# Kernel tuning notes

Hardware: AMD Instinct MI355X
Metric: run time of the kernel (lower is better)

## Reference

```python
import jax, jax.numpy as jnp
import numpy as np
from jax import lax


def ternarize(w):
    """Standard TWN ternarization with straight-through estimator.
    delta = 0.7*mean(|w|); alpha = mean(|w|) over kept entries; w_t = alpha*sign(w)*mask.
    """
    a = jnp.abs(w)
    delta = 0.7 * a.mean()
    mask = (a > delta).astype(w.dtype)
    alpha = (a * mask).sum() / jnp.maximum(mask.sum(), 1.0)
    wt = alpha * jnp.sign(w) * mask
    return w + lax.stop_gradient(wt - w)  # STE


def conv3x3(x, w, b):
    y = lax.conv_general_dilated(x, ternarize(w), window_strides=(1, 1),
                                 padding=((1, 1), (1, 1)),
                                 dimension_numbers=('NCHW', 'OIHW', 'NCHW'))
    return y + b[None, :, None, None]


def maxpool2(x):
    return lax.reduce_window(x, -jnp.inf, lax.max, (1, 1, 2, 2), (1, 1, 2, 2), 'VALID')


def setup_inputs() -> dict:
    key = jax.random.key(0)
    ks = jax.random.split(key, 11)
    s = lambda k, shape, scale: jax.random.normal(k, shape, dtype=jnp.float32) * scale
    return {
        'x':   s(ks[0], (1024, 3, 32, 32), 1.0),
        'w1':  s(ks[1], (64, 3, 3, 3), 0.1),
        'b1':  s(ks[2], (64,), 0.01),
        'w2':  s(ks[3], (128, 64, 3, 3), 0.05),
        'b2':  s(ks[4], (128,), 0.01),
        'w3':  s(ks[5], (256, 128, 3, 3), 0.03),
        'b3':  s(ks[6], (256,), 0.01),
        'wf1': s(ks[7], (256, 4096), 0.02),
        'bf1': s(ks[8], (256,), 0.01),
        'wf2': s(ks[9], (10, 256), 0.06),
        'bf2': s(ks[10], (10,), 0.01),
    }


def reference(x, w1, b1, w2, b2, w3, b3, wf1, bf1, wf2, bf2):
    x = maxpool2(jax.nn.relu(conv3x3(x, w1, b1)))   # [B,64,16,16]
    x = maxpool2(jax.nn.relu(conv3x3(x, w2, b2)))   # [B,128,8,8]
    x = maxpool2(jax.nn.relu(conv3x3(x, w3, b3)))   # [B,256,4,4]
    x = x.reshape(-1, 256 * 4 * 4)
    x = jax.nn.relu(x @ ternarize(wf1).T + bf1)     # [B,256]
    return x @ ternarize(wf2).T + bf2               # [B,10]
```

## Files before the change

### kernel.cpp

```cpp
#include <hip/hip_runtime.h>
#include <hip/hip_bf16.h>


typedef __attribute__((ext_vector_type(8))) short short8;
typedef __attribute__((ext_vector_type(4))) float f32x4;
typedef __attribute__((ext_vector_type(4))) int i32x4;

__device__ __forceinline__ unsigned short f2bf(float x) {
    unsigned u = __float_as_uint(x);
    return (unsigned short)((u + 0x7fffu + ((u >> 16) & 1u)) >> 16);
}
__device__ __forceinline__ float bf2f(unsigned short b) {
    return __uint_as_float(((unsigned)b) << 16);
}

#define WS_W1B   0
#define N_W1B    2048
#define WS_W2P   (WS_W1B + N_W1B)
#define N_W2P    (9*128*64)
#define WS_W3P   (WS_W2P + N_W2P)
#define N_W3P    (9*256*128)
#define WS_WTF1  (WS_W3P + N_W3P)
#define N_WTF1   (256*4096)
#define WS_WTF2  (WS_WTF1 + N_WTF1)
#define N_WTF2   (10*256)
#define WS_A1    (WS_WTF2 + N_WTF2)
#define N_A1     (1024*256*64)
#define WS_A2    (WS_A1 + N_A1)
#define N_A2     (1024*64*128)
#define WS_A3    (WS_A2 + N_A2)
#define N_A3     (1024*16*256)
#define WS_F1    (WS_A3 + N_A3)
#define N_F1     (1024*256)
#define WS_SCR   (WS_F1 + N_F1)

#define FC1_S    16

struct TernArgs {
    const float* w[6];
    int n[6];
};

__global__ void tern_stats1(TernArgs ta, double* __restrict__ scr) {
    const int wi = blockIdx.y;
    const float* __restrict__ w = ta.w[wi];
    const int n = ta.n[wi];
    __shared__ double red[4];
    const int lane = threadIdx.x & 63, wv = threadIdx.x >> 6;
    if (wi == 5) {
        float m = 0.f;
        for (int i = blockIdx.x * blockDim.x + threadIdx.x; i < n;
             i += gridDim.x * blockDim.x)
            m = fmaxf(m, fabsf(w[i]));
        #pragma unroll
        for (int off = 32; off > 0; off >>= 1)
            m = fmaxf(m, __shfl_down(m, off, 64));
        if (lane == 0) red[wv] = (double)m;
        __syncthreads();
        if (threadIdx.x == 0) {
            float mm = (float)fmax(fmax(red[0], red[1]), fmax(red[2], red[3]));
            atomicMax((int*)(scr + 20), __float_as_int(mm));
        }
        return;
    }
    double s = 0.0;
    for (int i = blockIdx.x * blockDim.x + threadIdx.x; i < n;
         i += gridDim.x * blockDim.x)
        s += (double)fabsf(w[i]);
    #pragma unroll
    for (int off = 32; off > 0; off >>= 1) s += __shfl_down(s, off, 64);
    if (lane == 0) red[wv] = s;
    __syncthreads();
    if (threadIdx.x == 0)
        atomicAdd(scr + wi * 4, red[0] + red[1] + red[2] + red[3]);
}

__global__ void tern_stats2(TernArgs ta, double* __restrict__ scr) {
    const int wi = blockIdx.y;
    const float* __restrict__ w = ta.w[wi];
    const int n = ta.n[wi];
    const float delta = (float)(0.7 * scr[wi * 4] / (double)n);
    double ms = 0.0, cnt = 0.0;
    for (int i = blockIdx.x * blockDim.x + threadIdx.x; i < n;
         i += gridDim.x * blockDim.x) {
        float a = fabsf(w[i]);
        if (a > delta) { ms += (double)a; cnt += 1.0; }
    }
    #pragma unroll
    for (int off = 32; off > 0; off >>= 1) {
        ms += __shfl_down(ms, off, 64);
        cnt += __shfl_down(cnt, off, 64);
    }
    __shared__ double redm[4], redc[4];
    const int lane = threadIdx.x & 63, wv = threadIdx.x >> 6;
    if (lane == 0) { redm[wv] = ms; redc[wv] = cnt; }
    __syncthreads();
    if (threadIdx.x == 0) {
        atomicAdd(scr + wi * 4 + 1, redm[0] + redm[1] + redm[2] + redm[3]);
        atomicAdd(scr + wi * 4 + 2, redc[0] + redc[1] + redc[2] + redc[3]);
    }
}

__global__ void tern_write_all(TernArgs ta, const double* __restrict__ scr,
                               signed char* __restrict__ w1b,
                               signed char* __restrict__ w2p8,
                               signed char* __restrict__ w3p8,
                               unsigned short* __restrict__ wtf1b,
                               float* __restrict__ wtf2) {
    const int wi = blockIdx.y;
    const float* __restrict__ w = ta.w[wi];
    const int n = ta.n[wi];
    const double* sc = scr + wi * 4;
    const float delta = (float)(0.7 * sc[0] / (double)n);
    const int i0 = blockIdx.x * blockDim.x + threadIdx.x;
    const int stride = gridDim.x * blockDim.x;

    if (wi == 0) {
        for (int i = i0; i < n; i += stride) {
            const int co = i / 27;
            const int kp = i % 27;
            float v = w[i];
            signed char s = (fabsf(v) > delta) ? (v > 0.0f ? 1 : -1) : 0;
            w1b[co * 64 + kp] = s;
            w1b[4096 + co * 64 + 32 + kp] = s;
        }
    } else if (wi == 4) {
        const double c = sc[2];
        const float alpha = (float)(sc[1] / (c > 1.0 ? c : 1.0));
        for (int i = i0; i < n; i += stride) {
            float v = w[i];
            wtf2[i] = (fabsf(v) > delta) ? (v > 0.0f ? alpha : -alpha) : 0.0f;
        }
    } else if (wi == 1 || wi == 2) {
        const int CIc = (wi == 1) ? 64 : 128;
        const int COc = (wi == 1) ? 128 : 256;
        signed char* dst = (wi == 1) ? w2p8 : w3p8;
        for (int i = i0; i < n; i += stride) {
            const int co = i / (CIc * 9);
            const int r = i % (CIc * 9);
            const int ci = r / 9, tap = r % 9;
            float v = w[i];
            signed char s = (fabsf(v) > delta) ? (v > 0.0f ? 1 : -1) : 0;
            dst[(tap * COc + co) * CIc + ci] = s;
        }
    } else {
        for (int i = i0; i < n; i += stride) {
            const int j = i >> 12;
            const int k = i & 4095;
            const int c = k >> 4, px = k & 15;
            float v = w[i];
            unsigned short s = (fabsf(v) > delta) ? (v > 0.0f ? 0x3f80 : 0xbf80) : 0;
            unsigned short* row = wtf1b + ((long)j << 13) + px * 512 + c;
            row[0] = s;
            row[256] = s;
        }
    }
}

__global__ __launch_bounds__(256) void conv1_i8(
        const float* __restrict__ x,
        const signed char* __restrict__ w1b,
        const float* __restrict__ bias,
        const double* __restrict__ scr,
        const int* __restrict__ amax_x,
        int* __restrict__ amax_out,
        float* __restrict__ y) {
    constexpr int PL = 3472;
    __shared__ __align__(16) char X[2 * PL];
    __shared__ float redm[4];

    const int b = blockIdx.x;
    const int tid = threadIdx.x;
    const float S = 32512.0f / fmaxf(__int_as_float(*amax_x), 1e-30f);

    for (int i = tid; i < 2 * PL / 16; i += 256)
        ((int4*)X)[i] = make_int4(0, 0, 0, 0);
    __syncthreads();

    for (int i = tid; i < 768; i += 256) {
        const float4 v = ((const float4*)(x + (long)b * 3072))[i];
        const int e = i * 4;
        const int ci = e >> 10;
        const int rem = e & 1023;
        const int h = rem >> 5, w = rem & 31;
        const int base = ci * 1156 + (h + 1) * 34 + (w + 1);
        const float f[4] = {v.x, v.y, v.z, v.w};
        #pragma unroll
        for (int j = 0; j < 4; j++) {
            const int q = __float2int_rn(f[j] * S);
            const int ql = (q << 24) >> 24;
            const int qh = (q - ql) >> 8;
            X[base + j] = (char)ql;
            X[PL + base + j] = (char)qh;
        }
    }
    __syncthreads();

    const int lane = tid & 63;
    const int wid = tid >> 6;
    const int lm = lane & 15;
    const int kg = lane >> 4;

    const int poff = (kg >= 2) ? PL : 0;
    int cst[16];
    #pragma unroll
    for (int j = 0; j < 16; j++) {
        const int kp = (kg & 1) * 16 + j;
        cst[j] = (kp < 27)
                     ? ((kp / 9) * 1156 + ((kp % 9) / 3) * 34 + (kp % 9) % 3)
                     : 0;
    }

    i32x4 BL[4], BH[4];
    #pragma unroll
    for (int nt = 0; nt < 4; nt++) {
        const int co = nt * 16 + lm;
        BL[nt] = *(const i32x4*)(w1b + (long)co * 64 + kg * 16);
        BH[nt] = *(const i32x4*)(w1b + 4096 + (long)co * 64 + kg * 16);
    }

    const double c2 = scr[2];
    const float alpha = (float)(scr[1] / (c2 > 1.0 ? c2 : 1.0));
    const float dq = alpha / S;
    float tmax = 0.f;
    float* yb = y + (long)b * 256 * 64;

    for (int tt = 0; tt < 16; ++tt) {
        const int t = wid * 16 + tt;
        const int pp = t * 4 + (lm >> 2);
        const int sub = lm & 3;
        const int h = 2 * (pp >> 4) + (sub >> 1);
        const int w = 2 * (pp & 15) + (sub & 1);
        const int base = poff + h * 34 + w;
        unsigned d[4] = {0u, 0u, 0u, 0u};
        #pragma unroll
        for (int j = 0; j < 16; j++) {
            const unsigned byte = (unsigned char)X[base + cst[j]];
            d[j >> 2] |= byte << ((j & 3) * 8);
        }
        i32x4 Af;
        Af[0] = (int)d[0]; Af[1] = (int)d[1];
        Af[2] = (int)d[2]; Af[3] = (int)d[3];

        const int opp = t * 4 + kg;
        float* yr = yb + (long)opp * 64;
        #pragma unroll
        for (int nt = 0; nt < 4; nt++) {
            i32x4 aL = 0, aH = 0;
            aL = __builtin_amdgcn_mfma_i32_16x16x64_i8(Af, BL[nt], aL, 0, 0, 0);
            aH = __builtin_amdgcn_mfma_i32_16x16x64_i8(Af, BH[nt], aH, 0, 0, 0);
            const int s0 = aH[0] * 256 + aL[0];
            const int s1 = aH[1] * 256 + aL[1];
            const int s2 = aH[2] * 256 + aL[2];
            const int s3 = aH[3] * 256 + aL[3];
            int sm = s0 > s1 ? s0 : s1;
            const int sn = s2 > s3 ? s2 : s3;
            sm = sm > sn ? sm : sn;
            const int co = nt * 16 + lm;
            const float o = fmaxf(dq * (float)sm + bias[co], 0.f);
            tmax = fmaxf(tmax, o);
            yr[co] = o;
        }
    }

    #pragma unroll
    for (int off = 32; off > 0; off >>= 1)
        tmax = fmaxf(tmax, __shfl_down(tmax, off, 64));
    if (lane == 0) redm[wid] = tmax;
    __syncthreads();
    if (tid == 0) {
        float m = fmaxf(fmaxf(redm[0], redm[1]), fmaxf(redm[2], redm[3]));
        atomicMax(amax_out, __float_as_int(m));
    }
}

template <int CI, int HI, int CO, int HB, int WM, int WN, bool INF32>
__global__ __launch_bounds__(256, 2) void conv_i8(
        const void* __restrict__ xin,
        const signed char* __restrict__ wp,
        const float* __restrict__ bias,
        const double* __restrict__ scr,
        const int* __restrict__ amax_in,
        int* __restrict__ amax_out,
        unsigned short* __restrict__ yout) {
    constexpr int CH8 = CI / 64;
    constexpr int NITER = 9 * CH8;
    constexpr int HR = HI / HB;
    constexpr int ROWS = HR + 2;
    constexpr int COLS = HI + 2;
    constexpr int NPIX = ROWS * COLS;
    constexpr int PSTR = NPIX * 64 + 32;
    constexpr int PO = HI / 2;
    constexpr int POR = HR / 2;
    constexpr int MT = 4, NT = 4;
    static_assert(WM * WN == 4, "4 waves");
    static_assert(WM * 64 == HR * HI, "M covers slab pixels");
    static_assert(WN * 64 == CO, "N covers all co");

    __shared__ __align__(16) char X[2 * CH8 * PSTR];
    __shared__ float redm[4];

    const int bimg = blockIdx.x / HB;
    const int hb = blockIdx.x % HB;
    const int tid = threadIdx.x;

    const float S = 32512.0f / fmaxf(__int_as_float(*amax_in), 1e-30f);

    constexpr int HALO = 2 * COLS + 2 * (ROWS - 2);
    for (int i = tid; i < HALO * 2 * CH8 * 4; i += 256) {
        const int u = i & 3;
        const int t = i >> 2;
        const int g = t % (2 * CH8);
        const int hp = t / (2 * CH8);
        int p;
        if (hp < COLS) p = hp;
        else if (hp < 2 * COLS) p = (ROWS - 1) * COLS + (hp - COLS);
        else {
            const int e = hp - 2 * COLS;
            p = (1 + (e >> 1)) * COLS + ((e & 1) ? (COLS - 1) : 0);
        }
        *(int4*)&X[g * PSTR + p * 64 + u * 16] = make_int4(0, 0, 0, 0);
    }

    for (int i = tid; i < ROWS * HI * (CI / 8); i += 256) {
        const int q8 = i % (CI / 8);
        const int t = i / (CI / 8);
        const int c = t % HI;
        const int r = t / HI;
        const int h = hb * HR + r - 1;
        if ((unsigned)h >= (unsigned)HI) continue;
        float f[8];
        if (INF32) {
            const float* pxr = (const float*)xin +
                ((long)(bimg * HI + h) * HI + c) * CI + q8 * 8;
            const float4 va = *(const float4*)(pxr);
            const float4 vb = *(const float4*)(pxr + 4);
            f[0] = va.x; f[1] = va.y; f[2] = va.z; f[3] = va.w;
            f[4] = vb.x; f[5] = vb.y; f[6] = vb.z; f[7] = vb.w;
        } else {
            const unsigned short* pxr = (const unsigned short*)xin +
                ((long)(bimg * HI + h) * HI + c) * (2 * CI);
            const uint4 vh = *(const uint4*)(pxr + q8 * 8);
            const uint4 vl = *(const uint4*)(pxr + CI + q8 * 8);
            const unsigned* hw = (const unsigned*)&vh;
            const unsigned* lw = (const unsigned*)&vl;
            #pragma unroll
            for (int j = 0; j < 8; j++) {
                const unsigned hu = (j & 1) ? (hw[j >> 1] >> 16)
                                            : (hw[j >> 1] & 0xffffu);
                const unsigned lu = (j & 1) ? (lw[j >> 1] >> 16)
                                            : (lw[j >> 1] & 0xffffu);
                f[j] = __uint_as_float(hu << 16) + __uint_as_float(lu << 16);
            }
        }
        unsigned pl0 = 0, pl1 = 0, ph0 = 0, ph1 = 0;
        #pragma unroll
        for (int j = 0; j < 8; j++) {
            const int qi = (int)(f[j] * S + 0.5f);
            const int ql = (qi << 24) >> 24;
            const int qh = (qi - ql) >> 8;
            const int sh = (j & 3) * 8;
            if (j < 4) {
                pl0 |= (unsigned)(ql & 255) << sh;
                ph0 |= (unsigned)(qh & 255) << sh;
            } else {
                pl1 |= (unsigned)(ql & 255) << sh;
                ph1 |= (unsigned)(qh & 255) << sh;
            }
        }
        const int p = r * COLS + c + 1;
        const int ch = q8 >> 3;
        const int cc = (q8 * 8) & 63;
        const int slot = ((cc >> 4) + (p >> 1)) & 3;
        const int base = p * 64 + slot * 16 + (cc & 15);
        *(uint2*)&X[ch * PSTR + base] = make_uint2(pl0, pl1);
        *(uint2*)&X[(CH8 + ch) * PSTR + base] = make_uint2(ph0, ph1);
    }
    __syncthreads();

    const int lane = tid & 63;
    const int wid = tid >> 6;
    const int wm = (WM == 1) ? 0 : (wid >> 1);
    const int wn = (WM == 1) ? wid : (wid & 1);
    const int lm = lane & 15;
    const int kg = lane >> 4;

    int pb[MT];
    #pragma unroll
    for (int mt = 0; mt < MT; mt++) {
        const int m = (wm * MT + mt) * 16 + lm;
        const int pp = m >> 2, sub = m & 3;
        const int lph = pp / PO, lpw = pp % PO;
        const int h = 2 * lph + (sub >> 1);
        const int w = 2 * lpw + (sub & 1);
        pb[mt] = h * COLS + w;
    }
    const signed char* bp[NT];
    #pragma unroll
    for (int nt = 0; nt < NT; nt++) {
        const int co = (wn * NT + nt) * 16 + lm;
        bp[nt] = wp + (long)co * CI + kg * 16;
    }

    i32x4 accL[MT][NT], accH[MT][NT];
    #pragma unroll
    for (int mt = 0; mt < MT; mt++)
        #pragma unroll
        for (int nt = 0; nt < NT; nt++) { accL[mt][nt] = 0; accH[mt][nt] = 0; }

    i32x4 Bb[2][NT];
    #pragma unroll
    for (int nt = 0; nt < NT; nt++) Bb[0][nt] = *(const i32x4*)(bp[nt]);

    #pragma unroll 2
    for (int it = 0; it < NITER; ++it) {
        const int cur = it & 1, nxt = cur ^ 1;
        if (it + 1 < NITER) {
            const int it1 = it + 1;
            const int tap = it1 / CH8, ch1 = it1 % CH8;
            const int woff = tap * CO * CI + ch1 * 64;
            #pragma unroll
            for (int nt = 0; nt < NT; nt++)
                Bb[nxt][nt] = *(const i32x4*)(bp[nt] + woff);
        }
        const int tap = it / CH8, ch = it % CH8;
        const int dtap = (tap / 3) * COLS + (tap % 3);
        int ao[MT];
        #pragma unroll
        for (int mt = 0; mt < MT; mt++) {
            const int p = pb[mt] + dtap;
            ao[mt] = p * 64 + (((kg + (p >> 1)) & 3) << 4);
        }
        {
            i32x4 Af[MT];
            #pragma unroll
            for (int mt = 0; mt < MT; mt++)
                Af[mt] = *(const i32x4*)&X[ch * PSTR + ao[mt]];
            #pragma unroll
            for (int mt = 0; mt < MT; mt++)
                #pragma unroll
                for (int nt = 0; nt < NT; nt++)
                    accL[mt][nt] = __builtin_amdgcn_mfma_i32_16x16x64_i8(
                        Af[mt], Bb[cur][nt], accL[mt][nt], 0, 0, 0);
        }
        {
            i32x4 Af[MT];
            #pragma unroll
            for (int mt = 0; mt < MT; mt++)
                Af[mt] = *(const i32x4*)&X[(CH8 + ch) * PSTR + ao[mt]];
            #pragma unroll
            for (int mt = 0; mt < MT; mt++)
                #pragma unroll
                for (int nt = 0; nt < NT; nt++)
                    accH[mt][nt] = __builtin_amdgcn_mfma_i32_16x16x64_i8(
                        Af[mt], Bb[cur][nt], accH[mt][nt], 0, 0, 0);
        }
    }

    const double c2 = scr[2];
    const float alpha = (float)(scr[1] / (c2 > 1.0 ? c2 : 1.0));
    const float dq = alpha / S;
    float tmax = 0.f;
    #pragma unroll
    for (int mt = 0; mt < MT; mt++) {
        const int pp = (wm * MT + mt) * 4 + kg;
        const int lph = pp / PO, lpw = pp % PO;
        const int gpp = (hb * POR + lph) * PO + lpw;
        unsigned short* yr = yout + ((long)bimg * (PO * PO) + gpp) * (2 * CO);
        #pragma unroll
        for (int nt = 0; nt < NT; nt++) {
            const int co = (wn * NT + nt) * 16 + lm;
            const i32x4 aL = accL[mt][nt], aH = accH[mt][nt];
            int s0 = aH[0] * 256 + aL[0];
            int s1 = aH[1] * 256 + aL[1];
            int s2 = aH[2] * 256 + aL[2];
            int s3 = aH[3] * 256 + aL[3];
            int sm = s0 > s1 ? s0 : s1;
            int sn = s2 > s3 ? s2 : s3;
            sm = sm > sn ? sm : sn;
            float o = fmaxf(dq * (float)sm + bias[co], 0.f);
            tmax = fmaxf(tmax, o);
            unsigned short hi = f2bf(o);
            unsigned short lo = f2bf(o - bf2f(hi));
            yr[co] = hi;
            yr[CO + co] = lo;
        }
    }
    if (amax_out) {
        #pragma unroll
        for (int off = 32; off > 0; off >>= 1)
            tmax = fmaxf(tmax, __shfl_down(tmax, off, 64));
        if (lane == 0) redm[wid] = tmax;
        __syncthreads();
        if (tid == 0) {
            float m = fmaxf(fmaxf(redm[0], redm[1]), fmaxf(redm[2], redm[3]));
            atomicMax(amax_out, __float_as_int(m));
        }
    }
}

template <int S>
__global__ __launch_bounds__(256) void fc1_mfma(
        const unsigned short* __restrict__ A,
        const unsigned short* __restrict__ Bw,
        float* __restrict__ parts) {
    constexpr int KCH = 8192 / S;
    constexpr int NSTEP = KCH / 32;
    const int m0 = blockIdx.x * 128;
    const int n0 = blockIdx.y * 128;
    const int s = blockIdx.z;
    const int tid = threadIdx.x;
    const int lane = tid & 63, wid = tid >> 6;
    const int wm = wid >> 1, wn = wid & 1;
    const int lm = lane & 15, kg = lane >> 4;

    const long k0 = (long)s * KCH + kg * 8;
    const unsigned short* ap[4];
    const unsigned short* bp[4];
    #pragma unroll
    for (int t = 0; t < 4; t++) {
        ap[t] = A + (long)(m0 + wm * 64 + t * 16 + lm) * 8192 + k0;
        bp[t] = Bw + (long)(n0 + wn * 64 + t * 16 + lm) * 8192 + k0;
    }

    f32x4 acc[4][4] = {};
    short8 Ab[2][4], Bb[2][4];
    #pragma unroll
    for (int t = 0; t < 4; t++) {
        Ab[0][t] = *(const short8*)(ap[t]);
        Bb[0][t] = *(const short8*)(bp[t]);
    }

    #pragma unroll 2
    for (int st = 0; st < NSTEP; ++st) {
        const int cur = st & 1, nxt = cur ^ 1;
        if (st + 1 < NSTEP) {
            const int off = (st + 1) * 32;
            #pragma unroll
            for (int t = 0; t < 4; t++) {
                Ab[nxt][t] = *(const short8*)(ap[t] + off);
                Bb[nxt][t] = *(const short8*)(bp[t] + off);
            }
        }
        #pragma unroll
        for (int mt = 0; mt < 4; mt++)
            #pragma unroll
            for (int nt = 0; nt < 4; nt++)
                acc[mt][nt] = __builtin_amdgcn_mfma_f32_16x16x32_bf16(
                    Ab[cur][mt], Bb[cur][nt], acc[mt][nt], 0, 0, 0);
    }

    #pragma unroll
    for (int mt = 0; mt < 4; mt++) {
        #pragma unroll
        for (int r = 0; r < 4; r++) {
            const int b = m0 + wm * 64 + mt * 16 + kg * 4 + r;
            #pragma unroll
            for (int nt = 0; nt < 4; nt++) {
                const int j = n0 + wn * 64 + nt * 16 + lm;
                parts[((long)s * 1024 + b) * 256 + j] = acc[mt][nt][r];
            }
        }
    }
}

template <int S>
__global__ __launch_bounds__(256) void fc2_fused(
        const float* __restrict__ parts,
        const double* __restrict__ scr,
        const float* __restrict__ bf1v,
        const float* __restrict__ wtf2,
        const float* __restrict__ bf2v,
        float* __restrict__ out) {
    __shared__ float sf[256];
    const int b = blockIdx.x;
    const int j = threadIdx.x;
    float s = 0.f;
    #pragma unroll
    for (int p = 0; p < S; p++)
        s += parts[(long)p * 262144 + (long)b * 256 + j];
    const double c2 = scr[2];
    const float alpha = (float)(scr[1] / (c2 > 1.0 ? c2 : 1.0));
    sf[j] = fmaxf(alpha * s + bf1v[j], 0.f);
    __syncthreads();
    const int lane = threadIdx.x & 63, wid = threadIdx.x >> 6;
    for (int k = wid; k < 10; k += 4) {
        const float* wr = wtf2 + k * 256;
        float acc = 0.f;
        #pragma unroll
        for (int t = 0; t < 4; t++)
            acc += sf[lane + t * 64] * wr[lane + t * 64];
        #pragma unroll
        for (int off = 32; off > 0; off >>= 1)
            acc += __shfl_down(acc, off, 64);
        if (lane == 0) out[(long)b * 10 + k] = acc + bf2v[k];
    }
}

extern "C" void kernel_launch(void* const* d_in, const int* in_sizes, int n_in,
                              void* d_out, int out_size, void* d_ws, size_t ws_size,
                              hipStream_t stream) {
    const float* x   = (const float*)d_in[0];
    const float* w1  = (const float*)d_in[1];
    const float* b1  = (const float*)d_in[2];
    const float* w2  = (const float*)d_in[3];
    const float* b2  = (const float*)d_in[4];
    const float* w3  = (const float*)d_in[5];
    const float* b3  = (const float*)d_in[6];
    const float* wf1 = (const float*)d_in[7];
    const float* bf1 = (const float*)d_in[8];
    const float* wf2 = (const float*)d_in[9];
    const float* bf2 = (const float*)d_in[10];
    float* out = (float*)d_out;
    float* ws = (float*)d_ws;

    const int B = 1024;

    signed char*    w1b   = (signed char*)(ws + WS_W1B);
    signed char*    w2p8  = (signed char*)(ws + WS_W2P);
    signed char*    w3p8  = (signed char*)(ws + WS_W3P);
    unsigned short* wtf1b = (unsigned short*)(ws + WS_WTF1);
    float*          wtf2  = ws + WS_WTF2;
    float*          a1f   = ws + WS_A1;
    unsigned short* a2p   = (unsigned short*)(ws + WS_A2);
    unsigned short* a3p   = (unsigned short*)(ws + WS_A3);
    double*         scr   = (double*)(ws + WS_SCR);
    int*            iscr  = (int*)(scr + 20);
    int*            amaxx = iscr;
    int*            amax1 = iscr + 1;
    int*            amax2 = iscr + 2;
    float*          parts = ws + WS_A1;

    hipMemsetAsync(scr, 0, 22 * sizeof(double), stream);
    hipMemsetAsync(w1b, 0, 8192, stream);

    TernArgs ta;
    ta.w[0] = w1;  ta.n[0] = 64 * 27;
    ta.w[1] = w2;  ta.n[1] = 128 * 64 * 9;
    ta.w[2] = w3;  ta.n[2] = 256 * 128 * 9;
    ta.w[3] = wf1; ta.n[3] = 256 * 4096;
    ta.w[4] = wf2; ta.n[4] = 10 * 256;
    ta.w[5] = x;   ta.n[5] = 1024 * 3 * 32 * 32;

    hipLaunchKernelGGL(tern_stats1, dim3(128, 6), dim3(256), 0, stream, ta, scr);
    hipLaunchKernelGGL(tern_stats2, dim3(128, 5), dim3(256), 0, stream, ta, scr);
    hipLaunchKernelGGL(tern_write_all, dim3(128, 5), dim3(256), 0, stream,
                       ta, scr, w1b, w2p8, w3p8, wtf1b, wtf2);

    hipLaunchKernelGGL(conv1_i8, dim3(B), dim3(256), 0, stream,
                       x, w1b, b1, scr + 0, amaxx, amax1, a1f);

    hipLaunchKernelGGL((conv_i8<64, 16, 128, 2, 2, 2, true>), dim3(B * 2),
                       dim3(256), 0, stream, a1f, w2p8, b2, scr + 4, amax1,
                       amax2, a2p);

    hipLaunchKernelGGL((conv_i8<128, 8, 256, 1, 1, 4, false>), dim3(B),
                       dim3(256), 0, stream, a2p, w3p8, b3, scr + 8, amax2,
                       (int*)nullptr, a3p);

    hipLaunchKernelGGL((fc1_mfma<FC1_S>), dim3(8, 2, FC1_S), dim3(256), 0, stream,
                       a3p, wtf1b, parts);

    hipLaunchKernelGGL((fc2_fused<FC1_S>), dim3(B), dim3(256), 0, stream,
                       parts, scr + 12, bf1, wtf2, bf2, out);
}
```

Baseline: 285.5 us.

## Stage conv input rows into LDS via global_load_lds before quantizing

```diff
diff --git a/kernel.cpp b/kernel.cpp
--- a/kernel.cpp
+++ b/kernel.cpp
@@ -5,6 +5,11 @@
 typedef __attribute__((ext_vector_type(8))) short short8;
 typedef __attribute__((ext_vector_type(4))) float f32x4;
 typedef __attribute__((ext_vector_type(4))) int i32x4;
+
+#define GLOAD_LDS16(g, l)                                              \
+    __builtin_amdgcn_global_load_lds(                                  \
+        (const __attribute__((address_space(1))) void*)(g),            \
+        (__attribute__((address_space(3))) void*)(l), 16, 0, 0)
 
 __device__ __forceinline__ unsigned short f2bf(float x) {
     unsigned u = __float_as_uint(x);
@@ -274,7 +279,7 @@
     }
 }
 
-template <int CI, int HI, int CO, int HB, int WM, int WN, bool INF32>
+template <int CI, int HI, int CO, int HB, int WM, int WN, bool INF32, int NPH>
 __global__ __launch_bounds__(256, 2) void conv_i8(
         const void* __restrict__ xin,
         const signed char* __restrict__ wp,
@@ -293,16 +298,22 @@
     constexpr int PO = HI / 2;
     constexpr int POR = HR / 2;
     constexpr int MT = 4, NT = 4;
+    constexpr int RWB = HI * CI * 4;
+    constexpr int RR = (ROWS + NPH - 1) / NPH;
     static_assert(WM * WN == 4, "4 waves");
     static_assert(WM * 64 == HR * HI, "M covers slab pixels");
     static_assert(WN * 64 == CO, "N covers all co");
+    static_assert(RWB == 4096, "row must be 4096 B");
 
     __shared__ __align__(16) char X[2 * CH8 * PSTR];
+    __shared__ __align__(16) char RAW[RR * RWB];
     __shared__ float redm[4];
 
     const int bimg = blockIdx.x / HB;
     const int hb = blockIdx.x % HB;
     const int tid = threadIdx.x;
+    const int lane = tid & 63;
+    const int wid = tid >> 6;
 
     const float S = 32512.0f / fmaxf(__int_as_float(*amax_in), 1e-30f);
 
@@ -322,64 +333,84 @@
         *(int4*)&X[g * PSTR + p * 64 + u * 16] = make_int4(0, 0, 0, 0);
     }
 
-    for (int i = tid; i < ROWS * HI * (CI / 8); i += 256) {
-        const int q8 = i % (CI / 8);
-        const int t = i / (CI / 8);
-        const int c = t % HI;
-        const int r = t / HI;
-        const int h = hb * HR + r - 1;
-        if ((unsigned)h >= (unsigned)HI) continue;
-        float f[8];
-        if (INF32) {
-            const float* pxr = (const float*)xin +
-                ((long)(bimg * HI + h) * HI + c) * CI + q8 * 8;
-            const float4 va = *(const float4*)(pxr);
-            const float4 vb = *(const float4*)(pxr + 4);
-            f[0] = va.x; f[1] = va.y; f[2] = va.z; f[3] = va.w;
-            f[4] = vb.x; f[5] = vb.y; f[6] = vb.z; f[7] = vb.w;
-        } else {
-            const unsigned short* pxr = (const unsigned short*)xin +
-                ((long)(bimg * HI + h) * HI + c) * (2 * CI);
-            const uint4 vh = *(const uint4*)(pxr + q8 * 8);
-            const uint4 vl = *(const uint4*)(pxr + CI + q8 * 8);
-            const unsigned* hw = (const unsigned*)&vh;
-            const unsigned* lw = (const unsigned*)&vl;
+    for (int ph = 0; ph < NPH; ph++) {
+        const int r0 = ph * RR;
+        const int rend = (r0 + RR < ROWS) ? (r0 + RR) : ROWS;
+        for (int r = r0; r < rend; r++) {
+            const int h = hb * HR + r - 1;
+            const int rl = r - r0;
+            if ((unsigned)h >= (unsigned)HI) {
+                *(int4*)&RAW[rl * RWB + tid * 16] = make_int4(0, 0, 0, 0);
+            } else if (wid == (r & 3)) {
+                const char* grow = (const char*)xin +
+                                   ((long)(bimg * HI + h)) * RWB;
+                #pragma unroll
+                for (int j = 0; j < RWB / 1024; j++)
+                    GLOAD_LDS16(grow + j * 1024 + lane * 16,
+                                &RAW[rl * RWB + j * 1024]);
+            }
+        }
+        __syncthreads();
+
+        const int NIT = (rend - r0) * HI * (CI / 8);
+        for (int i = tid; i < NIT; i += 256) {
+            const int q8 = i % (CI / 8);
+            const int t = i / (CI / 8);
+            const int c = t % HI;
+            const int rl = t / HI;
+            const int r = r0 + rl;
+            float f[8];
+            if (INF32) {
+                const float* pf =
+                    (const float*)&RAW[rl * RWB + c * (CI * 4) + q8 * 32];
+                const float4 va = *(const float4*)(pf);
+                const float4 vb = *(const float4*)(pf + 4);
+                f[0] = va.x; f[1] = va.y; f[2] = va.z; f[3] = va.w;
+                f[4] = vb.x; f[5] = vb.y; f[6] = vb.z; f[7] = vb.w;
+            } else {
+                const uint4 vh =
+                    *(const uint4*)&RAW[rl * RWB + c * (CI * 4) + q8 * 16];
+                const uint4 vl =
+                    *(const uint4*)&RAW[rl * RWB + c * (CI * 4) + CI * 2 +
+                                        q8 * 16];
+                const unsigned* hw = (const unsigned*)&vh;
+                const unsigned* lw = (const unsigned*)&vl;
+                #pragma unroll
+                for (int j = 0; j < 8; j++) {
+                    const unsigned hu = (j & 1) ? (hw[j >> 1] >> 16)
+                                                : (hw[j >> 1] & 0xffffu);
+                    const unsigned lu = (j & 1) ? (lw[j >> 1] >> 16)
+                                                : (lw[j >> 1] & 0xffffu);
+                    f[j] = __uint_as_float(hu << 16) +
+                           __uint_as_float(lu << 16);
+                }
+            }
+            unsigned pl0 = 0, pl1 = 0, ph0 = 0, ph1 = 0;
             #pragma unroll
             for (int j = 0; j < 8; j++) {
-                const unsigned hu = (j & 1) ? (hw[j >> 1] >> 16)
-                                            : (hw[j >> 1] & 0xffffu);
-                const unsigned lu = (j & 1) ? (lw[j >> 1] >> 16)
-                                            : (lw[j >> 1] & 0xffffu);
-                f[j] = __uint_as_float(hu << 16) + __uint_as_float(lu << 16);
+                const int qi = (int)(f[j] * S + 0.5f);
+                const int ql = (qi << 24) >> 24;
+                const int qh = (qi - ql) >> 8;
+                const int sh = (j & 3) * 8;
+                if (j < 4) {
+                    pl0 |= (unsigned)(ql & 255) << sh;
+                    ph0 |= (unsigned)(qh & 255) << sh;
+                } else {
+                    pl1 |= (unsigned)(ql & 255) << sh;
+                    ph1 |= (unsigned)(qh & 255) << sh;
+                }
             }
-        }
-        unsigned pl0 = 0, pl1 = 0, ph0 = 0, ph1 = 0;
-        #pragma unroll
-        for (int j = 0; j < 8; j++) {
-            const int qi = (int)(f[j] * S + 0.5f);
-            const int ql = (qi << 24) >> 24;
-            const int qh = (qi - ql) >> 8;
-            const int sh = (j & 3) * 8;
-            if (j < 4) {
-                pl0 |= (unsigned)(ql & 255) << sh;
-                ph0 |= (unsigned)(qh & 255) << sh;
-            } else {
-                pl1 |= (unsigned)(ql & 255) << sh;
-                ph1 |= (unsigned)(qh & 255) << sh;
-            }
-        }
-        const int p = r * COLS + c + 1;
-        const int ch = q8 >> 3;
-        const int cc = (q8 * 8) & 63;
-        const int slot = ((cc >> 4) + (p >> 1)) & 3;
-        const int base = p * 64 + slot * 16 + (cc & 15);
-        *(uint2*)&X[ch * PSTR + base] = make_uint2(pl0, pl1);
-        *(uint2*)&X[(CH8 + ch) * PSTR + base] = make_uint2(ph0, ph1);
-    }
-    __syncthreads();
-
-    const int lane = tid & 63;
-    const int wid = tid >> 6;
+            const int p = r * COLS + c + 1;
+            const int ch = q8 / (64 / 8);
+            const int cc = (q8 * 8) & 63;
+            const int slot = ((cc >> 4) + (p >> 1)) & 3;
+            const int base = p * 64 + slot * 16 + (cc & 15);
+            *(uint2*)&X[ch * PSTR + base] = make_uint2(pl0, pl1);
+            *(uint2*)&X[(CH8 + ch) * PSTR + base] = make_uint2(ph0, ph1);
+        }
+        __syncthreads();
+    }
+
     const int wm = (WM == 1) ? 0 : (wid >> 1);
     const int wn = (WM == 1) ? wid : (wid & 1);
     const int lm = lane & 15;
@@ -650,11 +681,11 @@
     hipLaunchKernelGGL(conv1_i8, dim3(B), dim3(256), 0, stream,
                        x, w1b, b1, scr + 0, amaxx, amax1, a1f);
 
-    hipLaunchKernelGGL((conv_i8<64, 16, 128, 2, 2, 2, true>), dim3(B * 2),
+    hipLaunchKernelGGL((conv_i8<64, 16, 128, 2, 2, 2, true, 1>), dim3(B * 2),
                        dim3(256), 0, stream, a1f, w2p8, b2, scr + 4, amax1,
                        amax2, a2p);
 
-    hipLaunchKernelGGL((conv_i8<128, 8, 256, 1, 1, 4, false>), dim3(B),
+    hipLaunchKernelGGL((conv_i8<128, 8, 256, 1, 1, 4, false, 2>), dim3(B),
                        dim3(256), 0, stream, a2p, w3p8, b3, scr + 8, amax2,
                        (int*)nullptr, a3p);
 
```

Measured after the change: 282.2 us. About the same (-1.2%).
